# Performance work log

Hardware: AMD Instinct MI355X
Metric: run time of the kernel (lower is better)

The kernel has to match this reference:

```python
import jax, jax.numpy as jnp
import numpy as np

CHANNELS = 256
REDUCTION = 4
REDUCED = max(1, CHANNELS // REDUCTION)  # 64


def setup_inputs() -> dict:
    key = jax.random.key(0)
    kx, kq, kk, kv, ko = jax.random.split(key, 5)
    B, C, H, W = 4, CHANNELS, 48, 48
    x = jax.random.normal(kx, (B, C, H, W), dtype=jnp.float32)
    # 1x1 conv weights (bias=False) for 3 q/k/v branches, stored as [3, reduced, C]
    wq = jax.random.normal(kq, (3, REDUCED, C), dtype=jnp.float32) * 0.05
    wk = jax.random.normal(kk, (3, REDUCED, C), dtype=jnp.float32) * 0.05
    wv = jax.random.normal(kv, (3, REDUCED, C), dtype=jnp.float32) * 0.05
    # output 1x1 conv: [C, 3*reduced]
    wo = jax.random.normal(ko, (C, 3 * REDUCED), dtype=jnp.float32) * 0.05
    return {"x": x, "wq": wq, "wk": wk, "wv": wv, "wo": wo}


def reference(x, wq, wk, wv, wo):
    B, C, H, W = x.shape
    N = H * W
    r = wq.shape[1]
    scale = 1.0 / float(r) ** 0.5
    xf = x.reshape(B, C, N)                      # [B, C, N]
    # 1x1 convs == channel matmuls; all 3 branches at once
    qs = jnp.einsum('irc,bcn->ibrn', wq, xf)     # [3, B, r, N]
    ks = jnp.einsum('irc,bcn->ibrn', wk, xf)
    vs = jnp.einsum('irc,bcn->ibrn', wv, xf)
    outs = []
    for i in range(3):                           # structural 3x3 nesting
        q = qs[i]                                # [B, r, N]
        acc = jnp.zeros((B, r, N), dtype=x.dtype)
        for j in range(3):
            # attn[b, n, m] = softmax_m(q[b,:,n] . k[b,:,m] / sqrt(r))
            attn = jax.nn.softmax(jnp.einsum('brn,brm->bnm', q, ks[j]) * scale, axis=-1)
            acc = acc + jnp.einsum('brm,bnm->brn', vs[j], attn)
        outs.append(acc)
    combined = jnp.concatenate(outs, axis=1)     # [B, 3r, N]
    out = jnp.einsum('cr,brn->bcn', wo, combined).reshape(B, C, H, W)
    return x * jax.nn.sigmoid(out)
```

## Files before the change

kernel.cpp:

```cpp
#include <hip/hip_runtime.h>


#define BB 4
#define CC 256
#define NN_ 2304
#define RR 64

#define OQ 0
#define OK_ 1769472
#define OV 3538944
#define OC 5308416
#define CSTR 1769472
#define FR_IB 147456
#define OXF 10616832
#define OWF 12976128
#define OWOF 13123584

typedef __bf16 bf16x8 __attribute__((ext_vector_type(8)));
typedef float f32x16 __attribute__((ext_vector_type(16)));
typedef unsigned short ushort8 __attribute__((ext_vector_type(8)));
typedef unsigned int uintx2 __attribute__((ext_vector_type(2)));
typedef unsigned int uintx4 __attribute__((ext_vector_type(4)));

#if __has_builtin(__builtin_amdgcn_exp2f)
#define EXP2(x) __builtin_amdgcn_exp2f(x)
#else
#define EXP2(x) exp2f(x)
#endif

__device__ __forceinline__ float bf2f(unsigned short s) {
    unsigned int u = ((unsigned int)s) << 16;
    return __builtin_bit_cast(float, u);
}
__device__ __forceinline__ unsigned int pk_bf16(float lo, float hi) {
    unsigned int r;
    asm("v_cvt_pk_bf16_f32 %0, %1, %2" : "=v"(r) : "v"(lo), "v"(hi));
    return r;
}

__global__ __launch_bounds__(256) void prep_kernel(
    const float* __restrict__ x, const float* __restrict__ wq,
    const float* __restrict__ wk, const float* __restrict__ wv,
    const float* __restrict__ wo, unsigned short* __restrict__ wsb)
{
    int bid = blockIdx.x;
    int t = threadIdx.x;
    if (bid < 9) {
        int s = bid;
        int type = s / 3, i = s % 3;
        const float* wsel = (type == 0) ? wq : (type == 1 ? wk : wv);
        const float scale = (type == 0) ? 0.18033688011112042f : 1.0f;
        unsigned short* dst = wsb + OWF + s * 16384;
        #pragma unroll
        for (int p = 0; p < 8; ++p) {
            int u = t + 256 * p;
            int ks = u >> 7, rb = (u >> 6) & 1, lo = u & 63;
            int row = rb * 32 + (lo & 31), c = ks * 16 + 8 * (lo >> 5);
            const float* src = wsel + ((i * 64 + row) * 256 + c);
            float4 f0 = *(const float4*)(src);
            float4 f1 = *(const float4*)(src + 4);
            uintx4 pwv = {pk_bf16(f0.x * scale, f0.y * scale),
                          pk_bf16(f0.z * scale, f0.w * scale),
                          pk_bf16(f1.x * scale, f1.y * scale),
                          pk_bf16(f1.z * scale, f1.w * scale)};
            *(uintx4*)(dst + (ks * 2 + rb) * 512 + lo * 8) = pwv;
        }
        return;
    }
    if (bid < 12) {
        int bb = bid - 9;
        #pragma unroll
        for (int p = 0; p < 8; ++p) {
            int u = t + 256 * p;
            int cg = bb * 32 + (u >> 6);
            int lane = u & 63;
            int ks = cg >> 3, rb = cg & 7;
            int row = rb * 32 + (lane & 31);
            int g = ks * 16 + 8 * (lane >> 5);
            const float* src = wo + row * 192 + g;
            float4 f0 = *(const float4*)(src);
            float4 f1 = *(const float4*)(src + 4);
            uintx4 pwv = {pk_bf16(f0.x, f0.y), pk_bf16(f0.z, f0.w),
                          pk_bf16(f1.x, f1.y), pk_bf16(f1.z, f1.w)};
            *(uintx4*)(wsb + OWOF + cg * 512 + lane * 8) = pwv;
        }
        return;
    }
    __shared__ __align__(16) float xs[64 * 132];
    int xb = bid - 12;
    int cq  = xb & 3;
    int nt2 = (xb >> 2) % 18;
    int b   = xb / 72;
    int c0 = cq * 64, n0 = nt2 * 128;
    #pragma unroll
    for (int p = 0; p < 8; ++p) {
        int u = t + 256 * p;
        int cl = u >> 5, nq = (u & 31) * 4;
        *(float4*)&xs[cl * 132 + nq] =
            *(const float4*)&x[((size_t)(b * CC + c0 + cl)) * NN_ + n0 + nq];
    }
    __syncthreads();
    unsigned short* xfb = wsb + OXF + ((size_t)b) * 72 * 16 * 512;
    #pragma unroll
    for (int p = 0; p < 4; ++p) {
        int u = t + 256 * p;
        int nb_l = u >> 8, ks_l = (u >> 6) & 3, lo = u & 63;
        int hh = lo >> 5, idx = lo & 31;
        int clb = ks_l * 16 + 8 * hh;
        int nn = nb_l * 32 + idx;
        unsigned int pw[4];
        #pragma unroll
        for (int d = 0; d < 4; ++d) {
            float a  = xs[(clb + 2 * d) * 132 + nn];
            float bb2 = xs[(clb + 2 * d + 1) * 132 + nn];
            pw[d] = pk_bf16(a, bb2);
        }
        int nb = nt2 * 4 + nb_l, ks = cq * 4 + ks_l;
        *(uintx4*)(xfb + (nb * 16 + ks) * 512 + lo * 8) =
            (uintx4){pw[0], pw[1], pw[2], pw[3]};
    }
}

__global__ __launch_bounds__(256) void proj_mfma(unsigned short* __restrict__ wsb)
{
    int bid = blockIdx.x;
    int s = bid / 72;
    int rem = bid % 72;
    int b = rem / 18, nb4 = rem % 18;
    int type = s / 3, i = s % 3;
    int t = threadIdx.x;
    int w = t >> 6, lane = t & 63;
    int lq = lane & 31, h = lane >> 5;
    int nb = nb4 * 4 + w;

    const unsigned short* wf = wsb + OWF + s * 16384 + lane * 8;
    const unsigned short* xf = wsb + OXF + ((size_t)(b * 72 + nb) * 16) * 512 + lane * 8;

    f32x16 o0 = {}, o1 = {};
    if (type < 2) {
        #pragma unroll
        for (int ks = 0; ks < 16; ++ks) {
            bf16x8 a0 = *(const bf16x8*)(wf + ks * 1024);
            bf16x8 a1 = *(const bf16x8*)(wf + ks * 1024 + 512);
            bf16x8 bx = *(const bf16x8*)(xf + ks * 512);
            o0 = __builtin_amdgcn_mfma_f32_32x32x16_bf16(a0, bx, o0, 0, 0, 0);
            o1 = __builtin_amdgcn_mfma_f32_32x32x16_bf16(a1, bx, o1, 0, 0, 0);
        }
    } else {
        #pragma unroll
        for (int ks = 0; ks < 16; ++ks) {
            bf16x8 a0 = *(const bf16x8*)(wf + ks * 1024);
            bf16x8 a1 = *(const bf16x8*)(wf + ks * 1024 + 512);
            bf16x8 bx = *(const bf16x8*)(xf + ks * 512);
            o0 = __builtin_amdgcn_mfma_f32_32x32x16_bf16(bx, a0, o0, 0, 0, 0);
            o1 = __builtin_amdgcn_mfma_f32_32x32x16_bf16(bx, a1, o1, 0, 0, 0);
        }
    }

    unsigned short* dstbase =
        wsb + ((type == 0) ? OQ : (type == 1 ? OK_ : OV)) +
        ((size_t)(i * 4 + b)) * FR_IB + nb * 2048;

    if (type < 2) {
        #pragma unroll
        for (int g = 0; g < 4; ++g) {
            int kd = 8 * g + 4 * h;
            int off = (kd >> 4) * 512 + ((kd >> 3) & 1) * 256 + lq * 8 + (kd & 7);
            *(uintx2*)(dstbase + off) =
                (uintx2){pk_bf16(o0[4 * g], o0[4 * g + 1]),
                         pk_bf16(o0[4 * g + 2], o0[4 * g + 3])};
            int kd2 = kd + 32;
            int off2 = (kd2 >> 4) * 512 + ((kd2 >> 3) & 1) * 256 + lq * 8 + (kd2 & 7);
            *(uintx2*)(dstbase + off2) =
                (uintx2){pk_bf16(o1[4 * g], o1[4 * g + 1]),
                         pk_bf16(o1[4 * g + 2], o1[4 * g + 3])};
        }
    } else {
        #pragma unroll
        for (int g = 0; g < 4; ++g) {
            int off = (g >> 1) * 1024 + (g & 1) * 256 + lq * 8 + 4 * h;
            *(uintx2*)(dstbase + off) =
                (uintx2){pk_bf16(o0[4 * g], o0[4 * g + 1]),
                         pk_bf16(o0[4 * g + 2], o0[4 * g + 3])};
            *(uintx2*)(dstbase + off + 512) =
                (uintx2){pk_bf16(o1[4 * g], o1[4 * g + 1]),
                         pk_bf16(o1[4 * g + 2], o1[4 * g + 3])};
        }
    }
}

__global__ __launch_bounds__(256, 5) void attn_kernel(unsigned short* __restrict__ wsb)
{
    __shared__ __align__(16) float fl[4352];

    int bid = blockIdx.x;
    int wid = (bid & 7) * 162 + (bid >> 3);
    int s12 = wid / 108;
    int rem = wid % 108;
    int j = s12 >> 2, b = s12 & 3;
    int i = rem / 36;
    int qp = rem % 36;
    int w = threadIdx.x >> 6;
    int ks = w & 1, qloc = w >> 1;
    int lane = threadIdx.x & 63;
    int lq = lane & 31;
    int h = lane >> 5;
    int q0 = (qp * 2 + qloc) * 32;
    int nt = q0 >> 5;

    const unsigned short* qtf = wsb + OQ + ((size_t)(i * 4 + b)) * FR_IB +
                                nt * 2048 + lane * 8;
    const unsigned short* kp = wsb + OK_ + ((size_t)(j * 4 + b)) * FR_IB +
                               (size_t)(ks * 36) * 2048 + lane * 8;
    const unsigned short* vp = wsb + OV + ((size_t)(j * 4 + b)) * FR_IB +
                               (size_t)(ks * 36) * 2048 + lane * 8;

    bf16x8 bq0 = *(const bf16x8*)(qtf + 0);
    bf16x8 bq1 = *(const bf16x8*)(qtf + 512);
    bf16x8 bq2 = *(const bf16x8*)(qtf + 1024);
    bf16x8 bq3 = *(const bf16x8*)(qtf + 1536);

    f32x16 o0 = {}, o1 = {};
    float l_loc = 0.f;

    bf16x8 k0 = *(const bf16x8*)(kp + 0 * 512);
    bf16x8 k1 = *(const bf16x8*)(kp + 1 * 512);
    bf16x8 k2 = *(const bf16x8*)(kp + 2 * 512);
    bf16x8 k3 = *(const bf16x8*)(kp + 3 * 512);

    for (int step = 0; step < 36; ++step) {
        const unsigned short* vb = vp + (size_t)step * 2048;
        bf16x8 v00 = *(const bf16x8*)(vb + 0 * 512);
        bf16x8 v10 = *(const bf16x8*)(vb + 1 * 512);
        bf16x8 v01 = *(const bf16x8*)(vb + 2 * 512);
        bf16x8 v11 = *(const bf16x8*)(vb + 3 * 512);

        f32x16 s = {};
        s = __builtin_amdgcn_mfma_f32_32x32x16_bf16(k0, bq0, s, 0, 0, 0);
        s = __builtin_amdgcn_mfma_f32_32x32x16_bf16(k1, bq1, s, 0, 0, 0);
        s = __builtin_amdgcn_mfma_f32_32x32x16_bf16(k2, bq2, s, 0, 0, 0);
        s = __builtin_amdgcn_mfma_f32_32x32x16_bf16(k3, bq3, s, 0, 0, 0);

        {
            int nx = (step + 1 < 36) ? (step + 1) : 0;
            const unsigned short* kb = kp + (size_t)nx * 2048;
            k0 = *(const bf16x8*)(kb + 0 * 512);
            k1 = *(const bf16x8*)(kb + 1 * 512);
            k2 = *(const bf16x8*)(kb + 2 * 512);
            k3 = *(const bf16x8*)(kb + 3 * 512);
        }

        #pragma unroll
        for (int r = 0; r < 16; ++r) s[r] = EXP2(s[r]);
        l_loc += ((s[0] + s[1]) + (s[2] + s[3])) + ((s[4] + s[5]) + (s[6] + s[7])) +
                 ((s[8] + s[9]) + (s[10] + s[11])) + ((s[12] + s[13]) + (s[14] + s[15]));

        {
            unsigned int a0 = pk_bf16(s[0], s[1]);
            unsigned int a1 = pk_bf16(s[2], s[3]);
            unsigned int b0 = pk_bf16(s[4], s[5]);
            unsigned int b1 = pk_bf16(s[6], s[7]);
            uintx2 r0 = __builtin_amdgcn_permlane32_swap(a0, b0, false, false);
            uintx2 r1 = __builtin_amdgcn_permlane32_swap(a1, b1, false, false);
            uintx4 pwv = {r0[0], r1[0], r0[1], r1[1]};
            bf16x8 pa = __builtin_bit_cast(bf16x8, pwv);
            o0 = __builtin_amdgcn_mfma_f32_32x32x16_bf16(v00, pa, o0, 0, 0, 0);
            o1 = __builtin_amdgcn_mfma_f32_32x32x16_bf16(v10, pa, o1, 0, 0, 0);
        }
        {
            unsigned int a0 = pk_bf16(s[8], s[9]);
            unsigned int a1 = pk_bf16(s[10], s[11]);
            unsigned int b0 = pk_bf16(s[12], s[13]);
            unsigned int b1 = pk_bf16(s[14], s[15]);
            uintx2 r0 = __builtin_amdgcn_permlane32_swap(a0, b0, false, false);
            uintx2 r1 = __builtin_amdgcn_permlane32_swap(a1, b1, false, false);
            uintx4 pwv = {r0[0], r1[0], r0[1], r1[1]};
            bf16x8 pa = __builtin_bit_cast(bf16x8, pwv);
            o0 = __builtin_amdgcn_mfma_f32_32x32x16_bf16(v01, pa, o0, 0, 0, 0);
            o1 = __builtin_amdgcn_mfma_f32_32x32x16_bf16(v11, pa, o1, 0, 0, 0);
        }
    }

    float l_full = l_loc + __shfl_xor(l_loc, 32);

    int off = qloc * 2112;
    if (ks == 1) {
        #pragma unroll
        for (int reg = 0; reg < 16; ++reg) {
            fl[off + reg * 64 + lane] = o0[reg];
            fl[off + 1024 + reg * 64 + lane] = o1[reg];
        }
        fl[off + 2048 + lane] = l_full;
    }
    __syncthreads();
    if (ks == 1) return;

    #pragma unroll
    for (int reg = 0; reg < 16; ++reg) {
        o0[reg] += fl[off + reg * 64 + lane];
        o1[reg] += fl[off + 1024 + reg * 64 + lane];
    }
    float l_tot = l_full + fl[off + 2048 + lane];
    __syncthreads();

    float inv = 1.f / l_tot;
    o0 *= inv; o1 *= inv;

    float* tw = fl + qloc * 2080;
    #pragma unroll
    for (int reg = 0; reg < 16; ++reg) {
        int rv = (reg & 3) + 8 * (reg >> 2) + 4 * h;
        tw[lq * 65 + rv] = o0[reg];
        tw[lq * 65 + 32 + rv] = o1[reg];
    }
    unsigned short* cb = wsb + OC + (size_t)j * CSTR +
                         ((size_t)((b * 72 + nt) * 12 + i * 4)) * 512;
    #pragma unroll
    for (int ksl = 0; ksl < 4; ++ksl) {
        const float* src = tw + lq * 65 + ksl * 16 + 8 * h;
        uintx4 pwv = {pk_bf16(src[0], src[1]), pk_bf16(src[2], src[3]),
                      pk_bf16(src[4], src[5]), pk_bf16(src[6], src[7])};
        *(uintx4*)(cb + ksl * 512 + lane * 8) = pwv;
    }
}

__global__ __launch_bounds__(256) void out_mfma(
    const float* __restrict__ x, const unsigned short* __restrict__ wsb,
    float* __restrict__ out)
{
    int bid = blockIdx.x;
    int ch = bid & 1;
    int nt = (bid >> 1) % 72;
    int b  = bid / 144;
    int n0 = nt * 32;
    int t = threadIdx.x;
    int w = t >> 6, lane = t & 63;
    int lq = lane & 31, h = lane >> 5;
    int rb = ch * 4 + w;

    const unsigned short* wof = wsb + OWOF + lane * 8;
    const unsigned short* cbase = wsb + OC +
        ((size_t)((b * 72 + nt) * 12)) * 512 + lane * 8;

    f32x16 acc = {};
    #pragma unroll
    for (int j = 0; j < 3; ++j) {
        const unsigned short* cj = cbase + (size_t)j * CSTR;
        #pragma unroll
        for (int ksx = 0; ksx < 12; ++ksx) {
            bf16x8 bx = *(const bf16x8*)(cj + ksx * 512);
            bf16x8 a0 = *(const bf16x8*)(wof + (ksx * 8 + rb) * 512);
            acc = __builtin_amdgcn_mfma_f32_32x32x16_bf16(a0, bx, acc, 0, 0, 0);
        }
    }

    int c0 = rb * 32;
    #pragma unroll
    for (int reg = 0; reg < 16; ++reg) {
        int c = c0 + (reg & 3) + 8 * (reg >> 2) + 4 * h;
        size_t idx = ((size_t)(b * CC + c)) * NN_ + n0 + lq;
        float sg = 1.f / (1.f + EXP2(acc[reg] * -1.44269504f));
        out[idx] = x[idx] * sg;
    }
}

extern "C" void kernel_launch(void* const* d_in, const int* in_sizes, int n_in,
                              void* d_out, int out_size, void* d_ws, size_t ws_size,
                              hipStream_t stream) {
    const float* x  = (const float*)d_in[0];
    const float* wq = (const float*)d_in[1];
    const float* wk = (const float*)d_in[2];
    const float* wv = (const float*)d_in[3];
    const float* wo = (const float*)d_in[4];
    unsigned short* wsb = (unsigned short*)d_ws;
    float* out = (float*)d_out;

    prep_kernel<<<300, 256, 0, stream>>>(x, wq, wk, wv, wo, wsb);
    proj_mfma<<<648, 256, 0, stream>>>(wsb);
    attn_kernel<<<1296, 256, 0, stream>>>(wsb);
    out_mfma<<<576, 256, 0, stream>>>(x, wsb, out);
}
```

Before: 98.76 us.

## Split attention key range across eight waves per query tile

Each block now handles a single 32-query tile with 8 waves, and each wave processes 9 of the 72 key tiles instead of 2 waves each handling 36. Partial outputs and row sums from 7 waves are reduced through shared memory by wave 0. This raises parallelism and shortens the per-wave serial loop, which should hide latency better. The cost is more reduction work, more shared memory, a doubled block count, and twice as many Q-fragment loads in total.

```diff
diff --git a/kernel.cpp b/kernel.cpp
--- a/kernel.cpp
+++ b/kernel.cpp
@@ -189,31 +189,29 @@
     }
 }
 
-__global__ __launch_bounds__(256, 5) void attn_kernel(unsigned short* __restrict__ wsb)
+__global__ __launch_bounds__(512, 4) void attn_kernel(unsigned short* __restrict__ wsb)
 {
-    __shared__ __align__(16) float fl[4352];
+    __shared__ __align__(16) float fl[7 * 2304];
 
     int bid = blockIdx.x;
-    int wid = (bid & 7) * 162 + (bid >> 3);
-    int s12 = wid / 108;
-    int rem = wid % 108;
+    int wid = (bid & 7) * 324 + (bid >> 3);
+    int s12 = wid / 216;
+    int rem = wid % 216;
     int j = s12 >> 2, b = s12 & 3;
-    int i = rem / 36;
-    int qp = rem % 36;
+    int i = rem / 72;
+    int qp = rem % 72;
     int w = threadIdx.x >> 6;
-    int ks = w & 1, qloc = w >> 1;
     int lane = threadIdx.x & 63;
     int lq = lane & 31;
     int h = lane >> 5;
-    int q0 = (qp * 2 + qloc) * 32;
-    int nt = q0 >> 5;
+    int q0 = qp * 32;
 
     const unsigned short* qtf = wsb + OQ + ((size_t)(i * 4 + b)) * FR_IB +
-                                nt * 2048 + lane * 8;
+                                qp * 2048 + lane * 8;
     const unsigned short* kp = wsb + OK_ + ((size_t)(j * 4 + b)) * FR_IB +
-                               (size_t)(ks * 36) * 2048 + lane * 8;
+                               (size_t)(w * 9) * 2048 + lane * 8;
     const unsigned short* vp = wsb + OV + ((size_t)(j * 4 + b)) * FR_IB +
-                               (size_t)(ks * 36) * 2048 + lane * 8;
+                               (size_t)(w * 9) * 2048 + lane * 8;
 
     bf16x8 bq0 = *(const bf16x8*)(qtf + 0);
     bf16x8 bq1 = *(const bf16x8*)(qtf + 512);
@@ -228,7 +226,7 @@
     bf16x8 k2 = *(const bf16x8*)(kp + 2 * 512);
     bf16x8 k3 = *(const bf16x8*)(kp + 3 * 512);
 
-    for (int step = 0; step < 36; ++step) {
+    for (int step = 0; step < 9; ++step) {
         const unsigned short* vb = vp + (size_t)step * 2048;
         bf16x8 v00 = *(const bf16x8*)(vb + 0 * 512);
         bf16x8 v10 = *(const bf16x8*)(vb + 1 * 512);
@@ -242,7 +240,7 @@
         s = __builtin_amdgcn_mfma_f32_32x32x16_bf16(k3, bq3, s, 0, 0, 0);
 
         {
-            int nx = (step + 1 < 36) ? (step + 1) : 0;
+            int nx = (step + 1 < 9) ? (step + 1) : 0;
             const unsigned short* kb = kp + (size_t)nx * 2048;
             k0 = *(const bf16x8*)(kb + 0 * 512);
             k1 = *(const bf16x8*)(kb + 1 * 512);
@@ -283,30 +281,39 @@
 
     float l_full = l_loc + __shfl_xor(l_loc, 32);
 
-    int off = qloc * 2112;
-    if (ks == 1) {
-        #pragma unroll
-        for (int reg = 0; reg < 16; ++reg) {
-            fl[off + reg * 64 + lane] = o0[reg];
-            fl[off + 1024 + reg * 64 + lane] = o1[reg];
-        }
-        fl[off + 2048 + lane] = l_full;
+    if (w > 0) {
+        float* sl = fl + (w - 1) * 2304 + lane * 36;
+        #pragma unroll
+        for (int g = 0; g < 4; ++g) {
+            *(float4*)(sl + 4 * g) =
+                make_float4(o0[4 * g], o0[4 * g + 1], o0[4 * g + 2], o0[4 * g + 3]);
+            *(float4*)(sl + 16 + 4 * g) =
+                make_float4(o1[4 * g], o1[4 * g + 1], o1[4 * g + 2], o1[4 * g + 3]);
+        }
+        sl[32] = l_full;
     }
     __syncthreads();
-    if (ks == 1) return;
-
-    #pragma unroll
-    for (int reg = 0; reg < 16; ++reg) {
-        o0[reg] += fl[off + reg * 64 + lane];
-        o1[reg] += fl[off + 1024 + reg * 64 + lane];
-    }
-    float l_tot = l_full + fl[off + 2048 + lane];
-    __syncthreads();
-
-    float inv = 1.f / l_tot;
+    if (w > 0) return;
+
+    #pragma unroll
+    for (int sidx = 0; sidx < 7; ++sidx) {
+        const float* sl = fl + sidx * 2304 + lane * 36;
+        #pragma unroll
+        for (int g = 0; g < 4; ++g) {
+            float4 a = *(const float4*)(sl + 4 * g);
+            float4 bb2 = *(const float4*)(sl + 16 + 4 * g);
+            o0[4 * g] += a.x; o0[4 * g + 1] += a.y;
+            o0[4 * g + 2] += a.z; o0[4 * g + 3] += a.w;
+            o1[4 * g] += bb2.x; o1[4 * g + 1] += bb2.y;
+            o1[4 * g + 2] += bb2.z; o1[4 * g + 3] += bb2.w;
+        }
+        l_full += sl[32];
+    }
+
+    float inv = 1.f / l_full;
     o0 *= inv; o1 *= inv;
 
-    float* tw = fl + qloc * 2080;
+    float* tw = fl;
     #pragma unroll
     for (int reg = 0; reg < 16; ++reg) {
         int rv = (reg & 3) + 8 * (reg >> 2) + 4 * h;
@@ -314,7 +321,7 @@
         tw[lq * 65 + 32 + rv] = o1[reg];
     }
     unsigned short* cb = wsb + OC + (size_t)j * CSTR +
-                         ((size_t)((b * 72 + nt) * 12 + i * 4)) * 512;
+                         ((size_t)((b * 72 + qp) * 12 + i * 4)) * 512;
     #pragma unroll
     for (int ksl = 0; ksl < 4; ++ksl) {
         const float* src = tw + lq * 65 + ksl * 16 + 8 * h;
@@ -377,6 +384,6 @@
 
     prep_kernel<<<300, 256, 0, stream>>>(x, wq, wk, wv, wo, wsb);
     proj_mfma<<<648, 256, 0, stream>>>(wsb);
-    attn_kernel<<<1296, 256, 0, stream>>>(wsb);
+    attn_kernel<<<2592, 512, 0, stream>>>(wsb);
     out_mfma<<<576, 256, 0, stream>>>(x, wsb, out);
 }
```

Result: no change. 97.35 us (-1.4%).

## Process two query tiles per wave and split keys four ways across waves

Applied to the files above, without the earlier changes.

Each wave now handles two 32-query tiles, reusing every loaded K and V fragment for both, and the four waves split the key range into quarters instead of two waves per query tile splitting it in halves. This halves K/V global/L2 traffic per query and interleaves two independent MFMA chains for latency hiding. In exchange, register pressure roughly doubles (occupancy hint lowered from 5 to 3 blocks), LDS use grows, and the cross-wave reduction needs three barriers instead of one. The final emit is serialized on a single wave.

```diff
diff --git a/kernel.cpp b/kernel.cpp
--- a/kernel.cpp
+++ b/kernel.cpp
@@ -189,9 +189,9 @@
     }
 }
 
-__global__ __launch_bounds__(256, 5) void attn_kernel(unsigned short* __restrict__ wsb)
+__global__ __launch_bounds__(256, 3) void attn_kernel(unsigned short* __restrict__ wsb)
 {
-    __shared__ __align__(16) float fl[4352];
+    __shared__ __align__(16) float fl[8448];
 
     int bid = blockIdx.x;
     int wid = (bid & 7) * 162 + (bid >> 3);
@@ -199,62 +199,38 @@
     int rem = wid % 108;
     int j = s12 >> 2, b = s12 & 3;
     int i = rem / 36;
-    int qp = rem % 36;
+    int qg = rem % 36;
     int w = threadIdx.x >> 6;
-    int ks = w & 1, qloc = w >> 1;
     int lane = threadIdx.x & 63;
     int lq = lane & 31;
     int h = lane >> 5;
-    int q0 = (qp * 2 + qloc) * 32;
-    int nt = q0 >> 5;
-
-    const unsigned short* qtf = wsb + OQ + ((size_t)(i * 4 + b)) * FR_IB +
-                                nt * 2048 + lane * 8;
+
+    const unsigned short* qbase = wsb + OQ + ((size_t)(i * 4 + b)) * FR_IB;
+    const unsigned short* qtfA = qbase + (size_t)(qg * 2) * 2048 + lane * 8;
+    const unsigned short* qtfB = qbase + (size_t)(qg * 2 + 1) * 2048 + lane * 8;
     const unsigned short* kp = wsb + OK_ + ((size_t)(j * 4 + b)) * FR_IB +
-                               (size_t)(ks * 36) * 2048 + lane * 8;
+                               (size_t)(w * 18) * 2048 + lane * 8;
     const unsigned short* vp = wsb + OV + ((size_t)(j * 4 + b)) * FR_IB +
-                               (size_t)(ks * 36) * 2048 + lane * 8;
-
-    bf16x8 bq0 = *(const bf16x8*)(qtf + 0);
-    bf16x8 bq1 = *(const bf16x8*)(qtf + 512);
-    bf16x8 bq2 = *(const bf16x8*)(qtf + 1024);
-    bf16x8 bq3 = *(const bf16x8*)(qtf + 1536);
-
-    f32x16 o0 = {}, o1 = {};
-    float l_loc = 0.f;
-
-    bf16x8 k0 = *(const bf16x8*)(kp + 0 * 512);
-    bf16x8 k1 = *(const bf16x8*)(kp + 1 * 512);
-    bf16x8 k2 = *(const bf16x8*)(kp + 2 * 512);
-    bf16x8 k3 = *(const bf16x8*)(kp + 3 * 512);
-
-    for (int step = 0; step < 36; ++step) {
-        const unsigned short* vb = vp + (size_t)step * 2048;
-        bf16x8 v00 = *(const bf16x8*)(vb + 0 * 512);
-        bf16x8 v10 = *(const bf16x8*)(vb + 1 * 512);
-        bf16x8 v01 = *(const bf16x8*)(vb + 2 * 512);
-        bf16x8 v11 = *(const bf16x8*)(vb + 3 * 512);
-
-        f32x16 s = {};
-        s = __builtin_amdgcn_mfma_f32_32x32x16_bf16(k0, bq0, s, 0, 0, 0);
-        s = __builtin_amdgcn_mfma_f32_32x32x16_bf16(k1, bq1, s, 0, 0, 0);
-        s = __builtin_amdgcn_mfma_f32_32x32x16_bf16(k2, bq2, s, 0, 0, 0);
-        s = __builtin_amdgcn_mfma_f32_32x32x16_bf16(k3, bq3, s, 0, 0, 0);
-
-        {
-            int nx = (step + 1 < 36) ? (step + 1) : 0;
-            const unsigned short* kb = kp + (size_t)nx * 2048;
-            k0 = *(const bf16x8*)(kb + 0 * 512);
-            k1 = *(const bf16x8*)(kb + 1 * 512);
-            k2 = *(const bf16x8*)(kb + 2 * 512);
-            k3 = *(const bf16x8*)(kb + 3 * 512);
-        }
-
+                               (size_t)(w * 18) * 2048 + lane * 8;
+
+    bf16x8 bqA0 = *(const bf16x8*)(qtfA + 0);
+    bf16x8 bqA1 = *(const bf16x8*)(qtfA + 512);
+    bf16x8 bqA2 = *(const bf16x8*)(qtfA + 1024);
+    bf16x8 bqA3 = *(const bf16x8*)(qtfA + 1536);
+    bf16x8 bqB0 = *(const bf16x8*)(qtfB + 0);
+    bf16x8 bqB1 = *(const bf16x8*)(qtfB + 512);
+    bf16x8 bqB2 = *(const bf16x8*)(qtfB + 1024);
+    bf16x8 bqB3 = *(const bf16x8*)(qtfB + 1536);
+
+    f32x16 o0a = {}, o1a = {}, o0b = {}, o1b = {};
+    float la = 0.f, lb = 0.f;
+
+    auto finish = [&](f32x16& s, f32x16& oo0, f32x16& oo1, float& ll,
+                      bf16x8 v00, bf16x8 v10, bf16x8 v01, bf16x8 v11) {
         #pragma unroll
         for (int r = 0; r < 16; ++r) s[r] = EXP2(s[r]);
-        l_loc += ((s[0] + s[1]) + (s[2] + s[3])) + ((s[4] + s[5]) + (s[6] + s[7])) +
-                 ((s[8] + s[9]) + (s[10] + s[11])) + ((s[12] + s[13]) + (s[14] + s[15]));
-
+        ll += ((s[0] + s[1]) + (s[2] + s[3])) + ((s[4] + s[5]) + (s[6] + s[7])) +
+              ((s[8] + s[9]) + (s[10] + s[11])) + ((s[12] + s[13]) + (s[14] + s[15]));
         {
             unsigned int a0 = pk_bf16(s[0], s[1]);
             unsigned int a1 = pk_bf16(s[2], s[3]);
@@ -264,8 +240,8 @@
             uintx2 r1 = __builtin_amdgcn_permlane32_swap(a1, b1, false, false);
             uintx4 pwv = {r0[0], r1[0], r0[1], r1[1]};
             bf16x8 pa = __builtin_bit_cast(bf16x8, pwv);
-            o0 = __builtin_amdgcn_mfma_f32_32x32x16_bf16(v00, pa, o0, 0, 0, 0);
-            o1 = __builtin_amdgcn_mfma_f32_32x32x16_bf16(v10, pa, o1, 0, 0, 0);
+            oo0 = __builtin_amdgcn_mfma_f32_32x32x16_bf16(v00, pa, oo0, 0, 0, 0);
+            oo1 = __builtin_amdgcn_mfma_f32_32x32x16_bf16(v10, pa, oo1, 0, 0, 0);
         }
         {
             unsigned int a0 = pk_bf16(s[8], s[9]);
@@ -276,52 +252,124 @@
             uintx2 r1 = __builtin_amdgcn_permlane32_swap(a1, b1, false, false);
             uintx4 pwv = {r0[0], r1[0], r0[1], r1[1]};
             bf16x8 pa = __builtin_bit_cast(bf16x8, pwv);
-            o0 = __builtin_amdgcn_mfma_f32_32x32x16_bf16(v01, pa, o0, 0, 0, 0);
-            o1 = __builtin_amdgcn_mfma_f32_32x32x16_bf16(v11, pa, o1, 0, 0, 0);
-        }
-    }
-
-    float l_full = l_loc + __shfl_xor(l_loc, 32);
-
-    int off = qloc * 2112;
-    if (ks == 1) {
+            oo0 = __builtin_amdgcn_mfma_f32_32x32x16_bf16(v01, pa, oo0, 0, 0, 0);
+            oo1 = __builtin_amdgcn_mfma_f32_32x32x16_bf16(v11, pa, oo1, 0, 0, 0);
+        }
+    };
+
+    bf16x8 k0 = *(const bf16x8*)(kp + 0 * 512);
+    bf16x8 k1 = *(const bf16x8*)(kp + 1 * 512);
+    bf16x8 k2 = *(const bf16x8*)(kp + 2 * 512);
+    bf16x8 k3 = *(const bf16x8*)(kp + 3 * 512);
+
+    for (int step = 0; step < 18; ++step) {
+        const unsigned short* vb = vp + (size_t)step * 2048;
+        bf16x8 v00 = *(const bf16x8*)(vb + 0 * 512);
+        bf16x8 v10 = *(const bf16x8*)(vb + 1 * 512);
+        bf16x8 v01 = *(const bf16x8*)(vb + 2 * 512);
+        bf16x8 v11 = *(const bf16x8*)(vb + 3 * 512);
+
+        f32x16 s = {};
+        s = __builtin_amdgcn_mfma_f32_32x32x16_bf16(k0, bqA0, s, 0, 0, 0);
+        s = __builtin_amdgcn_mfma_f32_32x32x16_bf16(k1, bqA1, s, 0, 0, 0);
+        s = __builtin_amdgcn_mfma_f32_32x32x16_bf16(k2, bqA2, s, 0, 0, 0);
+        s = __builtin_amdgcn_mfma_f32_32x32x16_bf16(k3, bqA3, s, 0, 0, 0);
+        finish(s, o0a, o1a, la, v00, v10, v01, v11);
+
+        f32x16 s2 = {};
+        s2 = __builtin_amdgcn_mfma_f32_32x32x16_bf16(k0, bqB0, s2, 0, 0, 0);
+        s2 = __builtin_amdgcn_mfma_f32_32x32x16_bf16(k1, bqB1, s2, 0, 0, 0);
+        s2 = __builtin_amdgcn_mfma_f32_32x32x16_bf16(k2, bqB2, s2, 0, 0, 0);
+        s2 = __builtin_amdgcn_mfma_f32_32x32x16_bf16(k3, bqB3, s2, 0, 0, 0);
+        {
+            int nx = (step + 1 < 18) ? (step + 1) : 0;
+            const unsigned short* kb = kp + (size_t)nx * 2048;
+            k0 = *(const bf16x8*)(kb + 0 * 512);
+            k1 = *(const bf16x8*)(kb + 1 * 512);
+            k2 = *(const bf16x8*)(kb + 2 * 512);
+            k3 = *(const bf16x8*)(kb + 3 * 512);
+        }
+        finish(s2, o0b, o1b, lb, v00, v10, v01, v11);
+    }
+
+    float la_f = la + __shfl_xor(la, 32);
+    float lb_f = lb + __shfl_xor(lb, 32);
+
+    if (w & 1) {
+        float* sl = fl + (w >> 1) * 4224;
         #pragma unroll
         for (int reg = 0; reg < 16; ++reg) {
-            fl[off + reg * 64 + lane] = o0[reg];
-            fl[off + 1024 + reg * 64 + lane] = o1[reg];
-        }
-        fl[off + 2048 + lane] = l_full;
+            sl[reg * 64 + lane] = o0a[reg];
+            sl[1024 + reg * 64 + lane] = o1a[reg];
+            sl[2048 + reg * 64 + lane] = o0b[reg];
+            sl[3072 + reg * 64 + lane] = o1b[reg];
+        }
+        sl[4096 + lane] = la_f;
+        sl[4160 + lane] = lb_f;
     }
     __syncthreads();
-    if (ks == 1) return;
+    if (!(w & 1)) {
+        const float* sl = fl + (w >> 1) * 4224;
+        #pragma unroll
+        for (int reg = 0; reg < 16; ++reg) {
+            o0a[reg] += sl[reg * 64 + lane];
+            o1a[reg] += sl[1024 + reg * 64 + lane];
+            o0b[reg] += sl[2048 + reg * 64 + lane];
+            o1b[reg] += sl[3072 + reg * 64 + lane];
+        }
+        la_f += sl[4096 + lane];
+        lb_f += sl[4160 + lane];
+    }
+    __syncthreads();
+    if (w == 2) {
+        float* sl = fl;
+        #pragma unroll
+        for (int reg = 0; reg < 16; ++reg) {
+            sl[reg * 64 + lane] = o0a[reg];
+            sl[1024 + reg * 64 + lane] = o1a[reg];
+            sl[2048 + reg * 64 + lane] = o0b[reg];
+            sl[3072 + reg * 64 + lane] = o1b[reg];
+        }
+        sl[4096 + lane] = la_f;
+        sl[4160 + lane] = lb_f;
+    }
+    __syncthreads();
+    if (w != 0) return;
 
     #pragma unroll
     for (int reg = 0; reg < 16; ++reg) {
-        o0[reg] += fl[off + reg * 64 + lane];
-        o1[reg] += fl[off + 1024 + reg * 64 + lane];
-    }
-    float l_tot = l_full + fl[off + 2048 + lane];
-    __syncthreads();
-
-    float inv = 1.f / l_tot;
-    o0 *= inv; o1 *= inv;
-
-    float* tw = fl + qloc * 2080;
-    #pragma unroll
-    for (int reg = 0; reg < 16; ++reg) {
-        int rv = (reg & 3) + 8 * (reg >> 2) + 4 * h;
-        tw[lq * 65 + rv] = o0[reg];
-        tw[lq * 65 + 32 + rv] = o1[reg];
-    }
-    unsigned short* cb = wsb + OC + (size_t)j * CSTR +
-                         ((size_t)((b * 72 + nt) * 12 + i * 4)) * 512;
-    #pragma unroll
-    for (int ksl = 0; ksl < 4; ++ksl) {
-        const float* src = tw + lq * 65 + ksl * 16 + 8 * h;
-        uintx4 pwv = {pk_bf16(src[0], src[1]), pk_bf16(src[2], src[3]),
-                      pk_bf16(src[4], src[5]), pk_bf16(src[6], src[7])};
-        *(uintx4*)(cb + ksl * 512 + lane * 8) = pwv;
-    }
+        o0a[reg] += fl[reg * 64 + lane];
+        o1a[reg] += fl[1024 + reg * 64 + lane];
+        o0b[reg] += fl[2048 + reg * 64 + lane];
+        o1b[reg] += fl[3072 + reg * 64 + lane];
+    }
+    la_f += fl[4096 + lane];
+    lb_f += fl[4160 + lane];
+
+    float inva = 1.f / la_f, invb = 1.f / lb_f;
+    o0a *= inva; o1a *= inva;
+    o0b *= invb; o1b *= invb;
+
+    auto emit = [&](f32x16 oo0, f32x16 oo1, int qp) {
+        float* tw = fl;
+        #pragma unroll
+        for (int reg = 0; reg < 16; ++reg) {
+            int rv = (reg & 3) + 8 * (reg >> 2) + 4 * h;
+            tw[lq * 65 + rv] = oo0[reg];
+            tw[lq * 65 + 32 + rv] = oo1[reg];
+        }
+        unsigned short* cb = wsb + OC + (size_t)j * CSTR +
+                             ((size_t)((b * 72 + qp) * 12 + i * 4)) * 512;
+        #pragma unroll
+        for (int ksl = 0; ksl < 4; ++ksl) {
+            const float* src = tw + lq * 65 + ksl * 16 + 8 * h;
+            uintx4 pwv = {pk_bf16(src[0], src[1]), pk_bf16(src[2], src[3]),
+                          pk_bf16(src[4], src[5]), pk_bf16(src[6], src[7])};
+            *(uintx4*)(cb + ksl * 512 + lane * 8) = pwv;
+        }
+    };
+    emit(o0a, o1a, qg * 2);
+    emit(o0b, o1b, qg * 2 + 1);
 }
 
 __global__ __launch_bounds__(256) void out_mfma(
```

Result: faster. 92.74 us (-6.1%).
